# Kernel optimization log

Measured on AMD Instinct MI355X. Metric: run time of the kernel, lower is better.

The kernel has to match this reference:

```python
import jax, jax.numpy as jnp
import numpy as np

N, F_DIM, H_DIM = 8192, 128, 128

def setup_inputs() -> dict:
    key = jax.random.key(0)
    ks = jax.random.split(key, 7)
    inp = {
        "input": jax.random.normal(ks[0], (N, F_DIM), dtype=jnp.float32),
        "wavelets": jax.random.normal(ks[1], (N, N), dtype=jnp.float32) / np.sqrt(N),
        "wavelets_inv": jax.random.normal(ks[2], (N, N), dtype=jnp.float32) / np.sqrt(N),
        # layer 1 params
        "W1": jax.random.uniform(ks[3], (F_DIM, H_DIM), dtype=jnp.float32,
                                 minval=-np.sqrt(6.0/(F_DIM+H_DIM)), maxval=np.sqrt(6.0/(F_DIM+H_DIM))),
        "f1": jax.random.uniform(ks[4], (N,), dtype=jnp.float32, minval=0.9, maxval=1.1),
        # layer 2 params
        "W2": jax.random.uniform(ks[5], (H_DIM, H_DIM), dtype=jnp.float32,
                                 minval=-np.sqrt(6.0/(H_DIM+H_DIM)), maxval=np.sqrt(6.0/(H_DIM+H_DIM))),
        "f2": jax.random.uniform(ks[6], (N,), dtype=jnp.float32, minval=0.9, maxval=1.1),
    }
    return inp

def _gwnn_layer(features, wavelets, wavelets_inv, W, filt):
    # torch: wavelets @ diag(filt) @ (wavelets_inv @ (features @ W))
    # diag(filt) matmul == column-wise scale of wavelets (broadcast elementwise)
    xw = features @ W                      # [N, out]
    spec = wavelets_inv @ xw               # [N, out] spectral-domain features
    spec = filt[:, None] * spec            # apply learnable diagonal filter
    return wavelets @ spec                 # [N, out]

def reference(input, wavelets, wavelets_inv, W1, f1, W2, f2):
    # eval mode: dropout is identity
    h1 = jax.nn.relu(_gwnn_layer(input, wavelets, wavelets_inv, W1, f1))
    out = _gwnn_layer(h1, wavelets, wavelets_inv, W2, f2)
    return out
```

## Files before the change

kernel.cpp:

```cpp
#include <hip/hip_runtime.h>
#include <hip/hip_bf16.h>
#include <stdint.h>


typedef __attribute__((ext_vector_type(4))) float f32x4;
typedef __attribute__((ext_vector_type(8))) short s16x8;
typedef __attribute__((ext_vector_type(4))) short s16x4;

#define DEVI static __device__ __forceinline__

DEVI short bf1(float x){ __bf16 h = (__bf16)x; return __builtin_bit_cast(short, h); }

DEVI s16x8 cvt8(f32x4 lo, f32x4 hi){
  s16x8 r;
#pragma unroll
  for (int i = 0; i < 4; ++i){ r[i] = bf1(lo[i]); r[4+i] = bf1(hi[i]); }
  return r;
}

DEVI void glds16(const void* g, void* l){
  __builtin_amdgcn_global_load_lds((const __attribute__((address_space(1))) void*)g,
                                   (__attribute__((address_space(3))) void*)l, 16, 0, 0);
}

template<int N> DEVI void waitvm(){
  if constexpr (N == 0)       asm volatile("s_waitcnt vmcnt(0)"  ::: "memory");
  else if constexpr (N == 5)  asm volatile("s_waitcnt vmcnt(5)"  ::: "memory");
  else if constexpr (N == 6)  asm volatile("s_waitcnt vmcnt(6)"  ::: "memory");
  else if constexpr (N == 8)  asm volatile("s_waitcnt vmcnt(8)"  ::: "memory");
  else if constexpr (N == 12) asm volatile("s_waitcnt vmcnt(12)" ::: "memory");
  else if constexpr (N == 16) asm volatile("s_waitcnt vmcnt(16)" ::: "memory");
  else if constexpr (N == 20) asm volatile("s_waitcnt vmcnt(20)" ::: "memory");
}

template<bool ABF, bool WCOPY>
__global__ __launch_bounds__(256, 1) void gemm_big(
    const void* __restrict__ Ap, const short* __restrict__ Btp,
    float* __restrict__ Pp, short* __restrict__ Acp, int K, int M)
{
  constexpr int BM = 128, BK = 64;
  constexpr int ASZ = ABF ? BM*BK*2 : BM*BK*4;
  constexpr int BSZ = 128*BK*2;
  constexpr int TSZ = ASZ + BSZ;
  constexpr int NBUF = ABF ? 4 : 3;
  constexpr int PRE  = ABF ? 3 : 2;
  __shared__ uint8_t lds[NBUF*TSZ];

  const int tid  = threadIdx.x;
  const int lane = tid & 63;
  const int wv   = tid >> 6;
  const int la   = lane & 15;
  const int g4   = lane >> 4;
  const int m0   = blockIdx.x * BM;
  const int kq   = blockIdx.y;
  const int K4   = K >> 2;
  const int kb   = kq * K4;

  const float* gAf = nullptr; const short* gAh = nullptr;
  int aoffg[8];
  if constexpr (!ABF){
    gAf = (const float*)Ap + (size_t)m0*K + kb;
#pragma unroll
    for (int j = 0; j < 8; ++j){
      const int rl = (wv<<5) + (j<<2) + (lane>>4);
      aoffg[j] = rl*K + (((lane&15) ^ (rl&15))<<2);
    }
  } else {
    gAh = (const short*)Ap + (size_t)m0*K + kb;
#pragma unroll
    for (int j = 0; j < 4; ++j){
      const int rl = (wv<<5) + (j<<3) + (lane>>3);
      aoffg[j] = rl*K + (((lane&7) ^ (rl&7))<<3);
    }
  }

  const int nb0 = (wv<<5) + (lane>>3);
  const short* gB0 = Btp + (size_t)(nb0    )*K + kb + (((lane&7)^(nb0&7))<<3);
  const short* gB1 = Btp + (size_t)(nb0+ 8 )*K + kb + (((lane&7)^(nb0&7))<<3);
  const short* gB2 = Btp + (size_t)(nb0+16 )*K + kb + (((lane&7)^(nb0&7))<<3);
  const short* gB3 = Btp + (size_t)(nb0+24 )*K + kb + (((lane&7)^(nb0&7))<<3);

  int aoff[2][2][2];
#pragma unroll
  for (int mi = 0; mi < 2; ++mi){
    const int r = (wv<<5) + mi*16 + la;
#pragma unroll
    for (int kf = 0; kf < 2; ++kf){
      if constexpr (!ABF){
        const int v0 = kf*8 + (g4<<1);
        aoff[mi][kf][0] = r*256 + (((v0  )^(r&15))<<4);
        aoff[mi][kf][1] = r*256 + (((v0+1)^(r&15))<<4);
      } else {
        const int u = kf*4 + g4;
        aoff[mi][kf][0] = r*128 + ((u^(r&7))<<4);
        aoff[mi][kf][1] = 0;
      }
    }
  }
  int boff[8][2];
#pragma unroll
  for (int ni = 0; ni < 8; ++ni){
    const int n = ni*16 + la;
#pragma unroll
    for (int kf = 0; kf < 2; ++kf){
      const int u = kf*4 + g4;
      boff[ni][kf] = n*128 + ((u^(n&7))<<4);
    }
  }

  short* Acw = nullptr;
  if constexpr (WCOPY)
    Acw = Acp + (size_t)(m0 + (wv<<5) + la)*K + kb + (g4<<3);

  f32x4 acc[2][8] = {};

  int kk = 0;
  int kc = 0;
  uint8_t* const lend = lds + NBUF*TSZ;
  uint8_t* bs = lds;
  uint8_t* bc = lds;

  auto STAGE = [&](){
    uint8_t* Ab = bs;
    uint8_t* Bb = bs + ASZ;
    if constexpr (!ABF){
#pragma unroll
      for (int j = 0; j < 8; ++j)
        glds16(gAf + aoffg[j] + kk, Ab + (wv<<13) + (j<<10));
    } else {
#pragma unroll
      for (int j = 0; j < 4; ++j)
        glds16(gAh + aoffg[j] + kk, Ab + (wv<<12) + (j<<10));
    }
    kk += BK;
    glds16(gB0, Bb + (wv<<12));
    glds16(gB1, Bb + (wv<<12) + 1024);
    glds16(gB2, Bb + (wv<<12) + 2048);
    glds16(gB3, Bb + (wv<<12) + 3072);
    gB0 += BK; gB1 += BK; gB2 += BK; gB3 += BK;
    bs += TSZ; if (bs == lend) bs = lds;
  };

  auto COMPUTE = [&](){
    const uint8_t* Ab = bc;
    const uint8_t* Bb = bc + ASZ;
#pragma unroll
    for (int kf = 0; kf < 2; ++kf){
      s16x8 a0, a1;
      if constexpr (!ABF){
        a0 = cvt8(*(const f32x4*)(Ab + aoff[0][kf][0]),
                  *(const f32x4*)(Ab + aoff[0][kf][1]));
        a1 = cvt8(*(const f32x4*)(Ab + aoff[1][kf][0]),
                  *(const f32x4*)(Ab + aoff[1][kf][1]));
        if constexpr (WCOPY){
          *(s16x8*)(Acw + kc + kf*32)            = a0;
          *(s16x8*)(Acw + (size_t)16*K + kc + kf*32) = a1;
        }
      } else {
        a0 = *(const s16x8*)(Ab + aoff[0][kf][0]);
        a1 = *(const s16x8*)(Ab + aoff[1][kf][0]);
      }
#pragma unroll
      for (int ni = 0; ni < 8; ++ni){
        s16x8 b = *(const s16x8*)(Bb + boff[ni][kf]);
        acc[0][ni] = __builtin_amdgcn_mfma_f32_16x16x32_bf16(a0, b, acc[0][ni], 0, 0, 0);
        acc[1][ni] = __builtin_amdgcn_mfma_f32_16x16x32_bf16(a1, b, acc[1][ni], 0, 0, 0);
      }
    }
    kc += BK;
    bc += TSZ; if (bc == lend) bc = lds;
  };

  const int ns = K4 >> 6;
  for (int s = 0; s < PRE && s < ns; ++s) STAGE();

  for (int t = 0; t < ns; ++t){
    if constexpr (ABF){
      if (t <= ns - 3)      waitvm<16>();
      else if (t == ns - 2) waitvm<8>();
      else                  waitvm<0>();
    } else if constexpr (WCOPY){
      if (t == 0)           waitvm<12>();
      else if (t == 1)      waitvm<16>();
      else if (t <= ns - 2) waitvm<20>();
      else                  waitvm<8>();
    } else {
      if (t < ns - 1) waitvm<12>(); else waitvm<0>();
    }
    __builtin_amdgcn_s_barrier();
    asm volatile("" ::: "memory");
    if (t + PRE < ns) STAGE();
    COMPUTE();
    asm volatile("" ::: "memory");
  }

  float* P = Pp + (size_t)kq * M * 128;
  const int rbase = m0 + (wv<<5) + (g4<<2);
#pragma unroll
  for (int mi = 0; mi < 2; ++mi)
#pragma unroll
    for (int ni = 0; ni < 8; ++ni)
#pragma unroll
      for (int r = 0; r < 4; ++r)
        P[(size_t)(rbase + mi*16 + r)*128 + ni*16 + la] = acc[mi][ni][r];
}

template<bool ABF>
__global__ __launch_bounds__(256, 1) void sgemm(
    const void* __restrict__ Ap, const short* __restrict__ Btp,
    void* __restrict__ Outp, int K, int M)
{
  constexpr int BM = 32, BN = 128, BK = 64;
  constexpr int ASZ = ABF ? BM*BK*2 : BM*BK*4;
  constexpr int BSZ = BN*BK*2;
  constexpr int TSZ = ASZ + BSZ;
  constexpr int NL  = ABF ? 5 : 6;
  constexpr int NBUF = 3, PRE = 2;
  __shared__ uint8_t lds[NBUF*TSZ];

  const int tid  = threadIdx.x;
  const int lane = tid & 63;
  const int wv   = tid >> 6;
  const int la   = lane & 15;
  const int g4   = lane >> 4;
  const int m0   = blockIdx.x * BM;

  const float* gA0 = nullptr; const float* gA1 = nullptr; const short* gAh = nullptr;
  if constexpr (!ABF){
    const float* Af = (const float*)Ap;
    int r0 = (wv<<3) + (lane>>4);
    int r1 = r0 + 4;
    gA0 = Af + (size_t)(m0+r0)*K + (((lane&15)^(r0&15))<<2);
    gA1 = Af + (size_t)(m0+r1)*K + (((lane&15)^(r1&15))<<2);
  } else {
    const short* Ah = (const short*)Ap;
    int r = (wv<<3) + (lane>>3);
    gAh = Ah + (size_t)(m0+r)*K + (((lane&7)^(r&7))<<3);
  }
  const int nb0 = (wv<<5) + (lane>>3);
  const short* gB0 = Btp + (size_t)(nb0    )*K + (((lane&7)^(nb0&7))<<3);
  const short* gB1 = Btp + (size_t)(nb0+ 8 )*K + (((lane&7)^(nb0&7))<<3);
  const short* gB2 = Btp + (size_t)(nb0+16 )*K + (((lane&7)^(nb0&7))<<3);
  const short* gB3 = Btp + (size_t)(nb0+24 )*K + (((lane&7)^(nb0&7))<<3);

  int aoff[2][2][2];
  int boff[2][2];
#pragma unroll
  for (int mi = 0; mi < 2; ++mi){
    const int r = mi*16 + la;
#pragma unroll
    for (int kf = 0; kf < 2; ++kf){
      if constexpr (!ABF){
        const int v0 = kf*8 + (g4<<1);
        aoff[mi][kf][0] = r*256 + (((v0  )^(r&15))<<4);
        aoff[mi][kf][1] = r*256 + (((v0+1)^(r&15))<<4);
      } else {
        const int u = kf*4 + g4;
        aoff[mi][kf][0] = r*128 + ((u^(r&7))<<4);
        aoff[mi][kf][1] = 0;
      }
    }
  }
#pragma unroll
  for (int ni = 0; ni < 2; ++ni){
    const int n = (wv<<5) + ni*16 + la;
#pragma unroll
    for (int kf = 0; kf < 2; ++kf){
      const int u = kf*4 + g4;
      boff[ni][kf] = n*128 + ((u^(n&7))<<4);
    }
  }

  f32x4 acc[2][2] = {};

  auto STAGE = [&](uint8_t* buf){
    uint8_t* Ab = buf;
    uint8_t* Bb = buf + ASZ;
    if constexpr (!ABF){
      glds16(gA0, Ab + (wv<<11));
      glds16(gA1, Ab + (wv<<11) + 1024);
      gA0 += BK; gA1 += BK;
    } else {
      glds16(gAh, Ab + (wv<<10));
      gAh += BK;
    }
    glds16(gB0, Bb + (wv<<12));
    glds16(gB1, Bb + (wv<<12) + 1024);
    glds16(gB2, Bb + (wv<<12) + 2048);
    glds16(gB3, Bb + (wv<<12) + 3072);
    gB0 += BK; gB1 += BK; gB2 += BK; gB3 += BK;
  };

  auto COMPUTE = [&](const uint8_t* buf){
    const uint8_t* Ab = buf;
    const uint8_t* Bb = buf + ASZ;
#pragma unroll
    for (int kf = 0; kf < 2; ++kf){
      s16x8 a0, a1, b0, b1;
      if constexpr (!ABF){
        a0 = cvt8(*(const f32x4*)(Ab + aoff[0][kf][0]), *(const f32x4*)(Ab + aoff[0][kf][1]));
        a1 = cvt8(*(const f32x4*)(Ab + aoff[1][kf][0]), *(const f32x4*)(Ab + aoff[1][kf][1]));
      } else {
        a0 = *(const s16x8*)(Ab + aoff[0][kf][0]);
        a1 = *(const s16x8*)(Ab + aoff[1][kf][0]);
      }
      b0 = *(const s16x8*)(Bb + boff[0][kf]);
      b1 = *(const s16x8*)(Bb + boff[1][kf]);
      acc[0][0] = __builtin_amdgcn_mfma_f32_16x16x32_bf16(a0, b0, acc[0][0], 0, 0, 0);
      acc[0][1] = __builtin_amdgcn_mfma_f32_16x16x32_bf16(a0, b1, acc[0][1], 0, 0, 0);
      acc[1][0] = __builtin_amdgcn_mfma_f32_16x16x32_bf16(a1, b0, acc[1][0], 0, 0, 0);
      acc[1][1] = __builtin_amdgcn_mfma_f32_16x16x32_bf16(a1, b1, acc[1][1], 0, 0, 0);
    }
  };

  const int ns = K >> 6;
  uint8_t* const lend = lds + NBUF*TSZ;
  uint8_t* bs = lds;
  uint8_t* bc = lds;
  for (int s = 0; s < PRE && s < ns; ++s){
    STAGE(bs);
    bs += TSZ; if (bs == lend) bs = lds;
  }
  for (int t = 0; t < ns; ++t){
    if (t < ns - 1) waitvm<NL>(); else waitvm<0>();
    __builtin_amdgcn_s_barrier();
    asm volatile("" ::: "memory");
    if (t + PRE < ns){
      STAGE(bs);
      bs += TSZ; if (bs == lend) bs = lds;
    }
    COMPUTE(bc);
    bc += TSZ; if (bc == lend) bc = lds;
    asm volatile("" ::: "memory");
  }

  const int mbase = m0 + (g4<<2);
  const int nc0   = (wv<<5) + la;
#pragma unroll
  for (int mi = 0; mi < 2; ++mi){
#pragma unroll
    for (int ni = 0; ni < 2; ++ni){
      s16x4 pk;
#pragma unroll
      for (int r = 0; r < 4; ++r) pk[r] = bf1(acc[mi][ni][r]);
      *(s16x4*)((short*)Outp + (size_t)(nc0 + (ni<<4))*M + (mbase + (mi<<4))) = pk;
    }
  }
}


__global__ __launch_bounds__(256) void red_t(
    const float* __restrict__ Pp, const float* __restrict__ fp,
    short* __restrict__ out, int M)
{
  __shared__ short t[128*65];
  const size_t S = (size_t)M*128;
  const int m0 = blockIdx.x * 64;
  const int tid = threadIdx.x;
#pragma unroll
  for (int it = 0; it < 8; ++it){
    const int idx = it*256 + tid;
    const int m = idx >> 5, nq = idx & 31;
    const float* base = Pp + (size_t)(m0+m)*128;
    f32x4 a = ((const f32x4*)(base      ))[nq];
    f32x4 b = ((const f32x4*)(base +   S))[nq];
    f32x4 c = ((const f32x4*)(base + 2*S))[nq];
    f32x4 d = ((const f32x4*)(base + 3*S))[nq];
    const float fv = fp[m0+m];
#pragma unroll
    for (int j = 0; j < 4; ++j)
      t[(nq*4+j)*65 + m] = bf1(fv * ((a[j] + b[j]) + (c[j] + d[j])));
  }
  __syncthreads();
#pragma unroll
  for (int it = 0; it < 8; ++it){
    const int idx = it*256 + tid;
    const int n = idx >> 4, mc = idx & 15;
    s16x4 v;
#pragma unroll
    for (int j = 0; j < 4; ++j) v[j] = t[n*65 + mc*4 + j];
    *(s16x4*)(out + (size_t)n*M + m0 + mc*4) = v;
  }
}

__global__ __launch_bounds__(256) void red_r(
    const float* __restrict__ Pp, short* __restrict__ out, int M)
{
  const size_t S = (size_t)M*128;
  const size_t i0 = (size_t)(blockIdx.x*256 + threadIdx.x) * 8;
  s16x8 v;
#pragma unroll
  for (int h = 0; h < 2; ++h){
    f32x4 a = *(const f32x4*)(Pp + i0 + 4*h);
    f32x4 b = *(const f32x4*)(Pp + i0 + 4*h + S);
    f32x4 c = *(const f32x4*)(Pp + i0 + 4*h + 2*S);
    f32x4 d = *(const f32x4*)(Pp + i0 + 4*h + 3*S);
#pragma unroll
    for (int j = 0; j < 4; ++j)
      v[4*h+j] = bf1(fmaxf((a[j] + b[j]) + (c[j] + d[j]), 0.0f));
  }
  *(s16x8*)(out + i0) = v;
}

__global__ __launch_bounds__(256) void red_f(
    const float* __restrict__ Pp, float* __restrict__ out, int M)
{
  const size_t S = (size_t)M*128;
  const size_t i0 = (size_t)(blockIdx.x*256 + threadIdx.x) * 4;
  f32x4 a = *(const f32x4*)(Pp + i0);
  f32x4 b = *(const f32x4*)(Pp + i0 + S);
  f32x4 c = *(const f32x4*)(Pp + i0 + 2*S);
  f32x4 d = *(const f32x4*)(Pp + i0 + 3*S);
  *(f32x4*)(out + i0) = (a + b) + (c + d);
}

__global__ void wtrans_k(const float* __restrict__ W1, const float* __restrict__ W2,
                         short* __restrict__ T1, short* __restrict__ T2){
  const int idx = blockIdx.x*256 + threadIdx.x;
  const int m = idx >> 14, rem = idx & 16383;
  const int n = rem >> 7, k = rem & 127;
  const float* W = m ? W2 : W1;
  short* T = m ? T2 : T1;
  T[n*128 + k] = bf1(W[k*128 + n]);
}

extern "C" void kernel_launch(void* const* d_in, const int* in_sizes, int n_in,
                              void* d_out, int out_size, void* d_ws, size_t ws_size,
                              hipStream_t stream){
  const float* input = (const float*)d_in[0];
  const float* wav   = (const float*)d_in[1];
  const float* winv  = (const float*)d_in[2];
  const float* W1    = (const float*)d_in[3];
  const float* f1    = (const float*)d_in[4];
  const float* W2    = (const float*)d_in[5];
  const float* f2    = (const float*)d_in[6];

  constexpr int M = 8192;
  uint8_t* ws = (uint8_t*)d_ws;
  short* W1T = (short*)(ws);
  short* W2T = (short*)(ws + (32<<10));
  short* XWT = (short*)(ws + (64<<10));
  short* SPT = (short*)(ws + (64<<10) + (2<<20));
  short* H1  = (short*)(ws + (64<<10) + (4<<20));
  float* P   = (float*)(ws + (64<<10) + (6<<20));
  short* WI16 = (short*)(ws + (64<<10) + (22<<20));
  short* WA16 = WI16 + (size_t)M*M;
  const size_t needed = (64<<10) + (size_t)(22<<20) + 2*(size_t)M*M*2;
  const bool big = (ws_size >= needed);

  dim3 b(256);
  dim3 gbig(M/128, 4);
  dim3 gns(M/32);
  dim3 grt(M/64);
  dim3 grr(M*128/(256*8));
  dim3 grf(M*128/(256*4));
  dim3 gt(128);

  wtrans_k<<<gt, b, 0, stream>>>(W1, W2, W1T, W2T);
  sgemm<false><<<gns, b, 0, stream>>>(input, W1T, XWT, 128, M);
  if (big){
    gemm_big<false,true ><<<gbig, b, 0, stream>>>(winv, XWT, P, WI16, M, M);
    red_t<<<grt, b, 0, stream>>>(P, f1, SPT, M);
    gemm_big<false,true ><<<gbig, b, 0, stream>>>(wav, SPT, P, WA16, M, M);
    red_r<<<grr, b, 0, stream>>>(P, H1, M);
    sgemm<true ><<<gns, b, 0, stream>>>(H1, W2T, XWT, 128, M);
    gemm_big<true ,false><<<gbig, b, 0, stream>>>(WI16, XWT, P, nullptr, M, M);
    red_t<<<grt, b, 0, stream>>>(P, f2, SPT, M);
    gemm_big<true ,false><<<gbig, b, 0, stream>>>(WA16, SPT, P, nullptr, M, M);
    red_f<<<grf, b, 0, stream>>>(P, (float*)d_out, M);
  } else {
    gemm_big<false,false><<<gbig, b, 0, stream>>>(winv, XWT, P, nullptr, M, M);
    red_t<<<grt, b, 0, stream>>>(P, f1, SPT, M);
    gemm_big<false,false><<<gbig, b, 0, stream>>>(wav, SPT, P, nullptr, M, M);
    red_r<<<grr, b, 0, stream>>>(P, H1, M);
    sgemm<true ><<<gns, b, 0, stream>>>(H1, W2T, XWT, 128, M);
    gemm_big<false,false><<<gbig, b, 0, stream>>>(winv, XWT, P, nullptr, M, M);
    red_t<<<grt, b, 0, stream>>>(P, f2, SPT, M);
    gemm_big<false,false><<<gbig, b, 0, stream>>>(wav, SPT, P, nullptr, M, M);
    red_f<<<grf, b, 0, stream>>>(P, (float*)d_out, M);
  }
}
```

Baseline: 354.8 us.

## Store bf16 wavelet copies in MFMA fragment-tiled layout for contiguous loads

The first-layer GEMMs now write the bf16 copies of the wavelet matrices in a blocked layout that matches the per-lane MFMA fragment order, so each wave's writes and the later second-layer reads are fully contiguous 16-byte chunks. The second-layer GEMMs read A from this tiled layout straight into LDS with no XOR swizzle and simpler address arithmetic. This is meant to remove strided row-major stores and loads across K and to simplify LDS addressing. The final wait in the copy-writing mode is tightened to vmcnt(0), which may add a small stall at the end of the loop.

```diff
diff --git a/kernel.cpp b/kernel.cpp
--- a/kernel.cpp
+++ b/kernel.cpp
@@ -33,14 +33,16 @@
   else if constexpr (N == 20) asm volatile("s_waitcnt vmcnt(20)" ::: "memory");
 }
 
-template<bool ABF, bool WCOPY>
+template<int MODE>
 __global__ __launch_bounds__(256, 1) void gemm_big(
     const void* __restrict__ Ap, const short* __restrict__ Btp,
-    float* __restrict__ Pp, short* __restrict__ Acp, int K, int M)
+    float* __restrict__ Pp, short* __restrict__ Cp, int K, int M)
 {
+  constexpr bool ABF = (MODE == 1);
+  constexpr bool WCP = (MODE == 0);
   constexpr int BM = 128, BK = 64;
-  constexpr int ASZ = ABF ? BM*BK*2 : BM*BK*4;
-  constexpr int BSZ = 128*BK*2;
+  constexpr int ASZ = ABF ? 16384 : 32768;
+  constexpr int BSZ = 16384;
   constexpr int TSZ = ASZ + BSZ;
   constexpr int NBUF = ABF ? 4 : 3;
   constexpr int PRE  = ABF ? 3 : 2;
@@ -51,12 +53,13 @@
   const int wv   = tid >> 6;
   const int la   = lane & 15;
   const int g4   = lane >> 4;
-  const int m0   = blockIdx.x * BM;
+  const int bx   = blockIdx.x;
   const int kq   = blockIdx.y;
+  const int m0   = bx * BM;
   const int K4   = K >> 2;
   const int kb   = kq * K4;
 
-  const float* gAf = nullptr; const short* gAh = nullptr;
+  const float* gAf = nullptr; const short* gAq = nullptr;
   int aoffg[8];
   if constexpr (!ABF){
     gAf = (const float*)Ap + (size_t)m0*K + kb;
@@ -66,12 +69,7 @@
       aoffg[j] = rl*K + (((lane&15) ^ (rl&15))<<2);
     }
   } else {
-    gAh = (const short*)Ap + (size_t)m0*K + kb;
-#pragma unroll
-    for (int j = 0; j < 4; ++j){
-      const int rl = (wv<<5) + (j<<3) + (lane>>3);
-      aoffg[j] = rl*K + (((lane&7) ^ (rl&7))<<3);
-    }
+    gAq = (const short*)Ap + (size_t)(kq*64 + bx)*262144 + (wv<<11) + (lane<<3);
   }
 
   const int nb0 = (wv<<5) + (lane>>3);
@@ -83,16 +81,15 @@
   int aoff[2][2][2];
 #pragma unroll
   for (int mi = 0; mi < 2; ++mi){
-    const int r = (wv<<5) + mi*16 + la;
 #pragma unroll
     for (int kf = 0; kf < 2; ++kf){
       if constexpr (!ABF){
+        const int r = (wv<<5) + mi*16 + la;
         const int v0 = kf*8 + (g4<<1);
         aoff[mi][kf][0] = r*256 + (((v0  )^(r&15))<<4);
         aoff[mi][kf][1] = r*256 + (((v0+1)^(r&15))<<4);
       } else {
-        const int u = kf*4 + g4;
-        aoff[mi][kf][0] = r*128 + ((u^(r&7))<<4);
+        aoff[mi][kf][0] = (wv<<12) + (((mi<<1)+kf)<<10) + (lane<<4);
         aoff[mi][kf][1] = 0;
       }
     }
@@ -108,9 +105,9 @@
     }
   }
 
-  short* Acw = nullptr;
-  if constexpr (WCOPY)
-    Acw = Acp + (size_t)(m0 + (wv<<5) + la)*K + kb + (g4<<3);
+  short* cw = nullptr;
+  if constexpr (WCP)
+    cw = Cp + (size_t)(kq*64 + bx)*262144 + (wv<<11) + (lane<<3);
 
   f32x4 acc[2][8] = {};
 
@@ -127,12 +124,13 @@
 #pragma unroll
       for (int j = 0; j < 8; ++j)
         glds16(gAf + aoffg[j] + kk, Ab + (wv<<13) + (j<<10));
+      kk += BK;
     } else {
 #pragma unroll
       for (int j = 0; j < 4; ++j)
-        glds16(gAh + aoffg[j] + kk, Ab + (wv<<12) + (j<<10));
-    }
-    kk += BK;
+        glds16(gAq + kk + (j<<9), Ab + (wv<<12) + (j<<10));
+      kk += 8192;
+    }
     glds16(gB0, Bb + (wv<<12));
     glds16(gB1, Bb + (wv<<12) + 1024);
     glds16(gB2, Bb + (wv<<12) + 2048);
@@ -152,9 +150,9 @@
                   *(const f32x4*)(Ab + aoff[0][kf][1]));
         a1 = cvt8(*(const f32x4*)(Ab + aoff[1][kf][0]),
                   *(const f32x4*)(Ab + aoff[1][kf][1]));
-        if constexpr (WCOPY){
-          *(s16x8*)(Acw + kc + kf*32)            = a0;
-          *(s16x8*)(Acw + (size_t)16*K + kc + kf*32) = a1;
+        if constexpr (WCP){
+          *(s16x8*)(cw + kc + (kf<<9))       = a0;
+          *(s16x8*)(cw + kc + ((2+kf)<<9))   = a1;
         }
       } else {
         a0 = *(const s16x8*)(Ab + aoff[0][kf][0]);
@@ -167,7 +165,7 @@
         acc[1][ni] = __builtin_amdgcn_mfma_f32_16x16x32_bf16(a1, b, acc[1][ni], 0, 0, 0);
       }
     }
-    kc += BK;
+    if constexpr (WCP) kc += 8192;
     bc += TSZ; if (bc == lend) bc = lds;
   };
 
@@ -179,11 +177,11 @@
       if (t <= ns - 3)      waitvm<16>();
       else if (t == ns - 2) waitvm<8>();
       else                  waitvm<0>();
-    } else if constexpr (WCOPY){
+    } else if constexpr (WCP){
       if (t == 0)           waitvm<12>();
       else if (t == 1)      waitvm<16>();
       else if (t <= ns - 2) waitvm<20>();
-      else                  waitvm<8>();
+      else                  waitvm<0>();
     } else {
       if (t < ns - 1) waitvm<12>(); else waitvm<0>();
     }
@@ -459,24 +457,24 @@
   wtrans_k<<<gt, b, 0, stream>>>(W1, W2, W1T, W2T);
   sgemm<false><<<gns, b, 0, stream>>>(input, W1T, XWT, 128, M);
   if (big){
-    gemm_big<false,true ><<<gbig, b, 0, stream>>>(winv, XWT, P, WI16, M, M);
+    gemm_big<0><<<gbig, b, 0, stream>>>(winv, XWT, P, WI16, M, M);
     red_t<<<grt, b, 0, stream>>>(P, f1, SPT, M);
-    gemm_big<false,true ><<<gbig, b, 0, stream>>>(wav, SPT, P, WA16, M, M);
+    gemm_big<0><<<gbig, b, 0, stream>>>(wav, SPT, P, WA16, M, M);
     red_r<<<grr, b, 0, stream>>>(P, H1, M);
     sgemm<true ><<<gns, b, 0, stream>>>(H1, W2T, XWT, 128, M);
-    gemm_big<true ,false><<<gbig, b, 0, stream>>>(WI16, XWT, P, nullptr, M, M);
+    gemm_big<1><<<gbig, b, 0, stream>>>(WI16, XWT, P, nullptr, M, M);
     red_t<<<grt, b, 0, stream>>>(P, f2, SPT, M);
-    gemm_big<true ,false><<<gbig, b, 0, stream>>>(WA16, SPT, P, nullptr, M, M);
+    gemm_big<1><<<gbig, b, 0, stream>>>(WA16, SPT, P, nullptr, M, M);
     red_f<<<grf, b, 0, stream>>>(P, (float*)d_out, M);
   } else {
-    gemm_big<false,false><<<gbig, b, 0, stream>>>(winv, XWT, P, nullptr, M, M);
+    gemm_big<2><<<gbig, b, 0, stream>>>(winv, XWT, P, nullptr, M, M);
     red_t<<<grt, b, 0, stream>>>(P, f1, SPT, M);
-    gemm_big<false,false><<<gbig, b, 0, stream>>>(wav, SPT, P, nullptr, M, M);
+    gemm_big<2><<<gbig, b, 0, stream>>>(wav, SPT, P, nullptr, M, M);
     red_r<<<grr, b, 0, stream>>>(P, H1, M);
     sgemm<true ><<<gns, b, 0, stream>>>(H1, W2T, XWT, 128, M);
-    gemm_big<false,false><<<gbig, b, 0, stream>>>(winv, XWT, P, nullptr, M, M);
+    gemm_big<2><<<gbig, b, 0, stream>>>(winv, XWT, P, nullptr, M, M);
     red_t<<<grt, b, 0, stream>>>(P, f2, SPT, M);
-    gemm_big<false,false><<<gbig, b, 0, stream>>>(wav, SPT, P, nullptr, M, M);
+    gemm_big<2><<<gbig, b, 0, stream>>>(wav, SPT, P, nullptr, M, M);
     red_f<<<grf, b, 0, stream>>>(P, (float*)d_out, M);
   }
 }
```

Measured after the change: 315.6 us. 1.12x faster.
